# Performance work log

Hardware: AMD Instinct MI355X
Metric: run time of the kernel (lower is better)

Reference implementation:

```python
import jax, jax.numpy as jnp
import numpy as np


def swish(x):
    return x * jax.nn.sigmoid(x)


def setup_inputs() -> dict:
    key = jax.random.key(0)
    ks = jax.random.split(key, 12)
    b, n, c, h, dg, hid = 4, 512, 256, 8, 6, 16

    def lin(k, i, o):
        return jax.random.normal(k, (i, o), jnp.float32) / np.float32(np.sqrt(i))

    return {
        "pairwise_g": jax.random.normal(ks[0], (b, n, n, dg), jnp.float32),
        "coset_functions": jax.random.normal(ks[1], (b, n, c), jnp.float32),
        "fc_q_w": lin(ks[2], c, c), "fc_q_b": jnp.zeros((c,), jnp.float32),
        "fc_k_w": lin(ks[3], c, c), "fc_k_b": jnp.zeros((c,), jnp.float32),
        "in_w": lin(ks[4], c, c), "in_b": jnp.zeros((c,), jnp.float32),
        "out_w": lin(ks[5], c, c), "out_b": jnp.zeros((c,), jnp.float32),
        "loc_w1": jax.random.normal(ks[6], (h, dg, hid), jnp.float32) / np.float32(np.sqrt(dg)),
        "loc_b1": jnp.zeros((h, hid), jnp.float32),
        "loc_w2": jax.random.normal(ks[7], (h, hid, hid), jnp.float32) / np.float32(np.sqrt(hid)),
        "loc_b2": jnp.zeros((h, hid), jnp.float32),
        "loc_w3": jax.random.normal(ks[8], (h, hid, 1), jnp.float32) / np.float32(np.sqrt(hid)),
        "loc_b3": jnp.zeros((h, 1), jnp.float32),
        "mask": jax.random.randint(ks[9], (4, 512), 0, 2) > 0,
    }


def reference(pairwise_g, coset_functions, fc_q_w, fc_q_b, fc_k_w, fc_k_b,
              in_w, in_b, out_w, out_b,
              loc_w1, loc_b1, loc_w2, loc_b2, loc_w3, loc_b3, mask):
    # nbhd_idx = arange(n) in the original (dense neighborhoods), so all
    # advanced-index gathers are identities and are expressed as broadcasts.
    b, n, c = coset_functions.shape
    h = loc_w1.shape[0]
    d = c // h

    # DotProductKernel: scores scaled by sqrt(embed_dim) = sqrt(c)
    Q = (coset_functions @ fc_q_w + fc_q_b).reshape(b, n, h, d)
    K = (coset_functions @ fc_k_w + fc_k_b).reshape(b, n, h, d)
    A_feat = jnp.einsum('bnhd,bmhd->bnmh', Q, K) / np.float32(np.sqrt(c))  # (b,n,m,h)

    # MultiheadWeightNet location kernel: per-head 3-layer MLP with swish
    # after every linear (LieConv-style LinearBNact blocks), out_dim=1.
    x = swish(jnp.einsum('bnmg,hgk->bnmhk', pairwise_g, loc_w1) + loc_b1)
    x = swish(jnp.einsum('bnmhk,hkj->bnmhj', x, loc_w2) + loc_b2)
    A_loc = swish(jnp.einsum('bnmhk,hko->bnmho', x, loc_w3) + loc_b3)[..., 0]  # (b,n,m,h)

    pre = A_loc + A_feat
    nbhd_mask = mask[:, None, :, None]          # mask over keys j: (b,1,m,1)
    pre = jnp.where(nbhd_mask, pre, jnp.float32(-1e38))
    att = jax.nn.softmax(pre, axis=2)           # softmax over neighbor dim m

    V = (coset_functions @ in_w + in_b).reshape(b, n, h, d)  # input_linear
    out = jnp.einsum('bnmh,bmhd->bnhd', att, V).reshape(b, n, c)
    return out @ out_w + out_b                  # output_linear; (b,n,c_out)
```

## Files before the change

### kernel.cpp

```cpp
#include <hip/hip_runtime.h>
#include <math.h>

namespace {

constexpr int kB = 4, kN = 512, kC = 256, kH = 8, kDG = 6, kHID = 16;

constexpr int S_QH = 20;
constexpr int S_BT = 20;
constexpr int S_AT = 516;

typedef _Float16 half2v __attribute__((ext_vector_type(2)));
typedef _Float16 half4v __attribute__((ext_vector_type(4)));
typedef float float4v __attribute__((ext_vector_type(4)));
typedef unsigned uint2v __attribute__((ext_vector_type(2)));

__device__ __forceinline__ float swishf(float x) {
    return x * __builtin_amdgcn_rcpf(1.0f + __expf(-x));
}

__device__ __forceinline__ unsigned pk16(float a, float b) {
    unsigned short ha = __builtin_bit_cast(unsigned short, (_Float16)a);
    unsigned short hb = __builtin_bit_cast(unsigned short, (_Float16)b);
    return (unsigned)ha | ((unsigned)hb << 16);
}

__device__ __forceinline__ unsigned pkrtz(float a, float b) {
    return __builtin_bit_cast(unsigned, __builtin_amdgcn_cvt_pkrtz(a, b));
}

__device__ __forceinline__ float4v mfma16(half4v a, half4v b, float4v c) {
    return __builtin_amdgcn_mfma_f32_16x16x16f16(a, b, c, 0, 0, 0);
}

__global__ __launch_bounds__(256) void k_qkvc(
    const float* __restrict__ x,
    const float* __restrict__ wq, const float* __restrict__ bq,
    const float* __restrict__ wk, const float* __restrict__ bk,
    const float* __restrict__ wv, const float* __restrict__ bv,
    unsigned* __restrict__ Qh, unsigned* __restrict__ Kh,
    unsigned* __restrict__ Vh,
    const unsigned char* __restrict__ mraw,
    int* __restrict__ list, int* __restrict__ meta) {
    const int t = threadIdx.x;

    if (blockIdx.x == 256) {
        __shared__ int s_isbool;
        if (t == 0) s_isbool = 0;
        __syncthreads();
        int found = 0;
        for (int i = t; i < kB * kN; i += 256)
            if ((i & 3) && mraw[i]) found = 1;
        if (found) atomicOr(&s_isbool, 1);
        __syncthreads();
        const int isb = s_isbool;
        const int b = t >> 6, lane = t & 63;
        const int* mi = (const int*)mraw;
        int base = 0;
        for (int c = 0; c < 8; ++c) {
            const int m = c * 64 + lane;
            const int idx = b * kN + m;
            const int valid = isb ? (mraw[idx] != 0) : (mi[idx] != 0);
            unsigned long long bal = __ballot(valid);
            int rank = (int)__popcll(bal & ((1ull << lane) - 1ull));
            if (valid) list[b * kN + base + rank] = m;
            base += (int)__popcll(bal);
        }
        for (int i = base + lane; i < kN; i += 64)
            list[b * kN + i] = (base == 0) ? i : 0;
        if (lane == 0) {
            meta[b] = (base == 0) ? kN : base;
            meta[4 + b] = (base == 0);
        }
        return;
    }

    __shared__ float sx[8][kC];
    const int r0 = blockIdx.x * 8;
    #pragma unroll
    for (int r = 0; r < 8; ++r) sx[r][t] = x[(r0 + r) * kC + t];
    __syncthreads();
    float aq[8] = {}, ak[8] = {}, av[8] = {};
    for (int k = 0; k < kC; ++k) {
        const float q = wq[k * kC + t];
        const float kk = wk[k * kC + t];
        const float v = wv[k * kC + t];
        #pragma unroll
        for (int r = 0; r < 8; ++r) {
            aq[r] += sx[r][k] * q;
            ak[r] += sx[r][k] * kk;
            av[r] += sx[r][k] * v;
        }
    }
    const float qb = bq[t], kb = bk[t], vb = bv[t];
    #pragma unroll
    for (int r = 0; r < 8; ++r) {
        const float qv = aq[r] + qb;
        const float kv = ak[r] + kb;
        const float vv = av[r] + vb;
        const float qn = __shfl_down(qv, 1);
        const float kn = __shfl_down(kv, 1);
        const float vn = __shfl_down(vv, 1);
        if ((t & 1) == 0) {
            Qh[(r0 + r) * (kC / 2) + (t >> 1)] = pk16(qv, qn);
            Kh[(r0 + r) * (kC / 2) + (t >> 1)] = pk16(kv, kn);
            Vh[(r0 + r) * (kC / 2) + (t >> 1)] = pk16(vv, vn);
        }
    }
}

__global__ __launch_bounds__(256, 4) void k_attn(
    const float* __restrict__ G,
    const unsigned* __restrict__ Qh,
    const unsigned* __restrict__ Kh,
    const unsigned* __restrict__ Vh,
    const float* __restrict__ w1, const float* __restrict__ b1,
    const float* __restrict__ w2, const float* __restrict__ b2,
    const float* __restrict__ w3, const float* __restrict__ b3,
    const int* __restrict__ list, const int* __restrict__ meta,
    float* __restrict__ out) {
    __shared__ __align__(16) unsigned sQh[kH * S_QH];
    __shared__ __align__(16) uint4 sG4[kN];
    __shared__ int sList[kN];
    __shared__ __align__(16) float sB1T[kH * S_BT];
    __shared__ __align__(16) float sB2T[kH * S_BT];
    __shared__ __align__(16) float sW3T[kH * S_BT];
    __shared__ float sB3[kH];
    __shared__ float sAtt[kH * S_AT];
    __shared__ float sInv[kH];

    const int bn = blockIdx.x;
    const int b = bn >> 9;
    const int t = threadIdx.x;
    const int l = t & 63;
    const int p = l & 15;
    const int s = l >> 4;
    const int wid = t >> 6;

    half4v a1f[kH], a2f[kH];
    #pragma unroll
    for (int h = 0; h < kH; ++h) {
        #pragma unroll
        for (int r = 0; r < 4; ++r) {
            const int k = 4 * s + r;
            a1f[h][r] = (k < kDG) ? (_Float16)w1[(h * kDG + k) * kHID + p]
                                  : (_Float16)0.f;
            a2f[h][r] = (_Float16)w2[(h * kHID + k) * kHID + p];
        }
    }

    if (t < kH * S_QH) {
        const int hh = t / S_QH, r = t % S_QH;
        sQh[t] = (r < 16) ? Qh[bn * (kC / 2) + hh * 16 + r] : 0u;
    }
    sList[t] = list[b * kN + t];
    sList[t + 256] = list[b * kN + t + 256];
    #pragma unroll 1
    for (int rep = 0; rep < 2; ++rep) {
        const int m = t + rep * 256;
        const float* gp = G + ((size_t)bn * kN + m) * kDG;
        uint4 gw;
        gw.x = pkrtz(gp[0], gp[1]);
        gw.y = pkrtz(gp[2], gp[3]);
        gw.z = pkrtz(gp[4], gp[5]);
        gw.w = 0;
        sG4[m] = gw;
    }
    if (t < 128) {
        const int hh = t >> 4, j = t & 15;
        sB1T[hh * S_BT + j] = b1[hh * kHID + j];
        sB2T[hh * S_BT + j] = b2[hh * kHID + j];
        sW3T[hh * S_BT + j] = w3[hh * kHID + j];
        if (j == 0) sB3[hh] = b3[hh];
    }
    const int nv = meta[b];
    const int allm = meta[4 + b];
    __syncthreads();

    const unsigned* khB = Kh + (size_t)(b * kN) * (kC / 2);
    const int ntiles = (nv + 15) >> 4;

    #pragma unroll
    for (int h = 0; h < kH; ++h) {
        const float4v bv1 = *(const float4v*)&sB1T[h * S_BT + s * 4];
        const float4v bv2 = *(const float4v*)&sB2T[h * S_BT + s * 4];
        const float4v w3f = *(const float4v*)&sW3T[h * S_BT + s * 4];
        half4v w3h;
        #pragma unroll
        for (int r = 0; r < 4; ++r) w3h[r] = (_Float16)w3f[r];
        const float b3s = sB3[h];
        const float4v b3v = {b3s, b3s, b3s, b3s};
        const uint2v q0u = {sQh[h * S_QH + 2 * s], sQh[h * S_QH + 2 * s + 1]};
        const uint2v q1u = {sQh[h * S_QH + 8 + 2 * s], sQh[h * S_QH + 9 + 2 * s]};
        const half4v qA0 = __builtin_bit_cast(half4v, q0u);
        const half4v qA1 = __builtin_bit_cast(half4v, q1u);

        #pragma unroll 1
        for (int tile = wid; tile < ntiles; tile += 4) {
            const int mcw = tile * 16 + p;
            const int mc = min(mcw, nv - 1);
            const int m = sList[mc];
            const unsigned* gp = (const unsigned*)&sG4[m];
            uint2v gu = {gp[(s & 1) * 2], gp[(s & 1) * 2 + 1]};
            if (s >= 2) { gu[0] = 0u; gu[1] = 0u; }
            const half4v bg = __builtin_bit_cast(half4v, gu);
            const float4v c1 = mfma16(a1f[h], bg, bv1);
            const uint2v x1u = {pkrtz(swishf(c1[0]), swishf(c1[1])),
                                pkrtz(swishf(c1[2]), swishf(c1[3]))};
            const float4v c2 = mfma16(a2f[h], __builtin_bit_cast(half4v, x1u), bv2);
            const uint2v x2u = {pkrtz(swishf(c2[0]), swishf(c2[1])),
                                pkrtz(swishf(c2[2]), swishf(c2[3]))};
            const float4v c3 = mfma16(w3h, __builtin_bit_cast(half4v, x2u), b3v);
            const unsigned* kr = khB + (size_t)m * (kC / 2) + h * 16 + 2 * s;
            const uint2v k0 = {kr[0], kr[1]};
            const uint2v k1 = {kr[8], kr[9]};
            float4v ca = {0.f, 0.f, 0.f, 0.f};
            ca = mfma16(qA0, __builtin_bit_cast(half4v, k0), ca);
            ca = mfma16(qA1, __builtin_bit_cast(half4v, k1), ca);
            const float pre = swishf(c3[0]) + ca[0] * 0.0625f;
            if (s == 0 && mcw < nv)
                sAtt[h * S_AT + mcw] = allm ? 0.f : pre;
        }
    }
    __syncthreads();

    {
        const int hg = t >> 5;
        const int lane = t & 31;
        float mx = -3.4e38f;
        for (int idx = lane; idx < nv; idx += 32)
            mx = fmaxf(mx, sAtt[hg * S_AT + idx]);
        #pragma unroll
        for (int off = 16; off; off >>= 1)
            mx = fmaxf(mx, __shfl_xor(mx, off));
        float ls = 0.f;
        for (int idx = lane; idx < nv; idx += 32) {
            const float e = __expf(sAtt[hg * S_AT + idx] - mx);
            sAtt[hg * S_AT + idx] = e;
            ls += e;
        }
        #pragma unroll
        for (int off = 16; off; off >>= 1)
            ls += __shfl_xor(ls, off);
        if (lane == 0) sInv[hg] = 1.0f / ls;
    }
    __syncthreads();

    {
        const int hg = t >> 5;
        const int dp = (t >> 1) & 15;
        const int par = t & 1;
        const unsigned* vbp = Vh + (size_t)(b * kN) * (kC / 2) + hg * 16 + dp;
        float alo = 0.f, ahi = 0.f, blo = 0.f, bhi = 0.f;
        int mc = par;
        for (; mc + 2 < nv; mc += 4) {
            const float aw0 = sAtt[hg * S_AT + mc];
            const float aw1 = sAtt[hg * S_AT + mc + 2];
            const half2v v0 = __builtin_bit_cast(half2v, vbp[(size_t)sList[mc] * (kC / 2)]);
            const half2v v1 = __builtin_bit_cast(half2v, vbp[(size_t)sList[mc + 2] * (kC / 2)]);
            alo += aw0 * (float)v0[0];
            ahi += aw0 * (float)v0[1];
            blo += aw1 * (float)v1[0];
            bhi += aw1 * (float)v1[1];
        }
        for (; mc < nv; mc += 2) {
            const float aw = sAtt[hg * S_AT + mc];
            const half2v vv = __builtin_bit_cast(half2v, vbp[(size_t)sList[mc] * (kC / 2)]);
            alo += aw * (float)vv[0];
            ahi += aw * (float)vv[1];
        }
        alo += blo; ahi += bhi;
        alo += __shfl_xor(alo, 1);
        ahi += __shfl_xor(ahi, 1);
        out[bn * kC + t] = (par ? ahi : alo) * sInv[hg];
    }
}

__global__ __launch_bounds__(256) void k_proj(
    const float* __restrict__ x,
    const float* __restrict__ w, const float* __restrict__ bias,
    float* __restrict__ y) {
    __shared__ float sx[8][kC];
    const int r0 = blockIdx.x * 8;
    const int t = threadIdx.x;
    #pragma unroll
    for (int r = 0; r < 8; ++r) sx[r][t] = x[(r0 + r) * kC + t];
    __syncthreads();
    float acc[8] = {};
    for (int k = 0; k < kC; ++k) {
        const float wv = w[k * kC + t];
        #pragma unroll
        for (int r = 0; r < 8; ++r) acc[r] += sx[r][k] * wv;
    }
    const float bb = bias[t];
    #pragma unroll
    for (int r = 0; r < 8; ++r) y[(r0 + r) * kC + t] = acc[r] + bb;
}

}

extern "C" void kernel_launch(void* const* d_in, const int* in_sizes, int n_in,
                              void* d_out, int out_size, void* d_ws, size_t ws_size,
                              hipStream_t stream) {
    (void)in_sizes; (void)n_in; (void)out_size; (void)ws_size;
    const float* G  = (const float*)d_in[0];
    const float* cf = (const float*)d_in[1];
    const float* wq = (const float*)d_in[2];
    const float* bq = (const float*)d_in[3];
    const float* wk = (const float*)d_in[4];
    const float* bk = (const float*)d_in[5];
    const float* wv = (const float*)d_in[6];
    const float* bv = (const float*)d_in[7];
    const float* wo = (const float*)d_in[8];
    const float* bo = (const float*)d_in[9];
    const float* w1 = (const float*)d_in[10];
    const float* b1 = (const float*)d_in[11];
    const float* w2 = (const float*)d_in[12];
    const float* b2 = (const float*)d_in[13];
    const float* w3 = (const float*)d_in[14];
    const float* b3 = (const float*)d_in[15];
    const unsigned char* mraw = (const unsigned char*)d_in[16];

    const int rows = kB * kN;
    unsigned* Qh = (unsigned*)d_ws;
    unsigned* Kh = Qh + (size_t)rows * (kC / 2);
    unsigned* Vh = Kh + (size_t)rows * (kC / 2);
    float* O = (float*)(Vh + (size_t)rows * (kC / 2));
    int* list = (int*)(O + (size_t)rows * kC);
    int* meta = list + rows;

    k_qkvc<<<257, 256, 0, stream>>>(cf, wq, bq, wk, bk, wv, bv,
                                    Qh, Kh, Vh, mraw, list, meta);
    k_attn<<<rows, 256, 0, stream>>>(G, Qh, Kh, Vh, w1, b1, w2, b2, w3, b3,
                                     list, meta, O);
    k_proj<<<rows / 8, 256, 0, stream>>>(O, wo, bo, (float*)d_out);
}
```

Before: 264.1 us.

## Split projection kernels across column halves and interleave two tiles in attention loop

The QKV and output projection kernels now launch twice as many blocks, each handling 128 output columns for 4 rows per thread group, which raises grid parallelism on a large GPU. The attention score loop processes two 16-key tiles per iteration with interleaved MFMA chains and hoisted K loads, exposing more instruction-level parallelism to hide latency. The cost is more register pressure in the attention kernel and duplicated x loads across the column-split blocks.

```diff
diff --git a/kernel.cpp b/kernel.cpp
--- a/kernel.cpp
+++ b/kernel.cpp
@@ -43,7 +43,7 @@
     int* __restrict__ list, int* __restrict__ meta) {
     const int t = threadIdx.x;
 
-    if (blockIdx.x == 256) {
+    if (blockIdx.x == 512) {
         __shared__ int s_isbool;
         if (t == 0) s_isbool = 0;
         __syncthreads();
@@ -75,25 +75,30 @@
     }
 
     __shared__ float sx[8][kC];
-    const int r0 = blockIdx.x * 8;
+    const int r0 = (blockIdx.x >> 1) * 8;
+    const int c0 = (blockIdx.x & 1) * 128;
+    const int col = t & 127;
+    const int g = t >> 7;
     #pragma unroll
     for (int r = 0; r < 8; ++r) sx[r][t] = x[(r0 + r) * kC + t];
     __syncthreads();
-    float aq[8] = {}, ak[8] = {}, av[8] = {};
+    float aq[4] = {}, ak[4] = {}, av[4] = {};
     for (int k = 0; k < kC; ++k) {
-        const float q = wq[k * kC + t];
-        const float kk = wk[k * kC + t];
-        const float v = wv[k * kC + t];
-        #pragma unroll
-        for (int r = 0; r < 8; ++r) {
-            aq[r] += sx[r][k] * q;
-            ak[r] += sx[r][k] * kk;
-            av[r] += sx[r][k] * v;
-        }
-    }
-    const float qb = bq[t], kb = bk[t], vb = bv[t];
-    #pragma unroll
-    for (int r = 0; r < 8; ++r) {
+        const float q = wq[k * kC + c0 + col];
+        const float kk = wk[k * kC + c0 + col];
+        const float v = wv[k * kC + c0 + col];
+        #pragma unroll
+        for (int r = 0; r < 4; ++r) {
+            const float xs = sx[g * 4 + r][k];
+            aq[r] += xs * q;
+            ak[r] += xs * kk;
+            av[r] += xs * v;
+        }
+    }
+    const float qb = bq[c0 + col], kb = bk[c0 + col], vb = bv[c0 + col];
+    #pragma unroll
+    for (int r = 0; r < 4; ++r) {
+        const int row = r0 + g * 4 + r;
         const float qv = aq[r] + qb;
         const float kv = ak[r] + kb;
         const float vv = av[r] + vb;
@@ -101,9 +106,10 @@
         const float kn = __shfl_down(kv, 1);
         const float vn = __shfl_down(vv, 1);
         if ((t & 1) == 0) {
-            Qh[(r0 + r) * (kC / 2) + (t >> 1)] = pk16(qv, qn);
-            Kh[(r0 + r) * (kC / 2) + (t >> 1)] = pk16(kv, kn);
-            Vh[(r0 + r) * (kC / 2) + (t >> 1)] = pk16(vv, vn);
+            const int ci = (c0 + col) >> 1;
+            Qh[row * (kC / 2) + ci] = pk16(qv, qn);
+            Kh[row * (kC / 2) + ci] = pk16(kv, kn);
+            Vh[row * (kC / 2) + ci] = pk16(vv, vn);
         }
     }
 }
@@ -195,30 +201,50 @@
         const half4v qA1 = __builtin_bit_cast(half4v, q1u);
 
         #pragma unroll 1
-        for (int tile = wid; tile < ntiles; tile += 4) {
-            const int mcw = tile * 16 + p;
-            const int mc = min(mcw, nv - 1);
-            const int m = sList[mc];
-            const unsigned* gp = (const unsigned*)&sG4[m];
-            uint2v gu = {gp[(s & 1) * 2], gp[(s & 1) * 2 + 1]};
-            if (s >= 2) { gu[0] = 0u; gu[1] = 0u; }
-            const half4v bg = __builtin_bit_cast(half4v, gu);
-            const float4v c1 = mfma16(a1f[h], bg, bv1);
-            const uint2v x1u = {pkrtz(swishf(c1[0]), swishf(c1[1])),
-                                pkrtz(swishf(c1[2]), swishf(c1[3]))};
-            const float4v c2 = mfma16(a2f[h], __builtin_bit_cast(half4v, x1u), bv2);
-            const uint2v x2u = {pkrtz(swishf(c2[0]), swishf(c2[1])),
-                                pkrtz(swishf(c2[2]), swishf(c2[3]))};
-            const float4v c3 = mfma16(w3h, __builtin_bit_cast(half4v, x2u), b3v);
-            const unsigned* kr = khB + (size_t)m * (kC / 2) + h * 16 + 2 * s;
-            const uint2v k0 = {kr[0], kr[1]};
-            const uint2v k1 = {kr[8], kr[9]};
-            float4v ca = {0.f, 0.f, 0.f, 0.f};
-            ca = mfma16(qA0, __builtin_bit_cast(half4v, k0), ca);
-            ca = mfma16(qA1, __builtin_bit_cast(half4v, k1), ca);
-            const float pre = swishf(c3[0]) + ca[0] * 0.0625f;
-            if (s == 0 && mcw < nv)
-                sAtt[h * S_AT + mcw] = allm ? 0.f : pre;
+        for (int tile = wid; tile < ntiles; tile += 8) {
+            const int mcwA = tile * 16 + p;
+            const int mcwB = mcwA + 64;
+            const int mcA = min(mcwA, nv - 1);
+            const int mcB = min(mcwB, nv - 1);
+            const int mA = sList[mcA];
+            const int mB = sList[mcB];
+            const unsigned* krA = khB + (size_t)mA * (kC / 2) + h * 16 + 2 * s;
+            const unsigned* krB = khB + (size_t)mB * (kC / 2) + h * 16 + 2 * s;
+            const uint2v k0A = {krA[0], krA[1]};
+            const uint2v k1A = {krA[8], krA[9]};
+            const uint2v k0B = {krB[0], krB[1]};
+            const uint2v k1B = {krB[8], krB[9]};
+            const unsigned* gpA = (const unsigned*)&sG4[mA];
+            const unsigned* gpB = (const unsigned*)&sG4[mB];
+            uint2v guA = {gpA[(s & 1) * 2], gpA[(s & 1) * 2 + 1]};
+            uint2v guB = {gpB[(s & 1) * 2], gpB[(s & 1) * 2 + 1]};
+            if (s >= 2) { guA[0] = 0u; guA[1] = 0u; guB[0] = 0u; guB[1] = 0u; }
+            const half4v bgA = __builtin_bit_cast(half4v, guA);
+            const half4v bgB = __builtin_bit_cast(half4v, guB);
+            float4v caA = {0.f, 0.f, 0.f, 0.f};
+            float4v caB = {0.f, 0.f, 0.f, 0.f};
+            caA = mfma16(qA0, __builtin_bit_cast(half4v, k0A), caA);
+            caB = mfma16(qA0, __builtin_bit_cast(half4v, k0B), caB);
+            caA = mfma16(qA1, __builtin_bit_cast(half4v, k1A), caA);
+            caB = mfma16(qA1, __builtin_bit_cast(half4v, k1B), caB);
+            const float4v c1A = mfma16(a1f[h], bgA, bv1);
+            const float4v c1B = mfma16(a1f[h], bgB, bv1);
+            const uint2v x1uA = {pkrtz(swishf(c1A[0]), swishf(c1A[1])),
+                                 pkrtz(swishf(c1A[2]), swishf(c1A[3]))};
+            const uint2v x1uB = {pkrtz(swishf(c1B[0]), swishf(c1B[1])),
+                                 pkrtz(swishf(c1B[2]), swishf(c1B[3]))};
+            const float4v c2A = mfma16(a2f[h], __builtin_bit_cast(half4v, x1uA), bv2);
+            const float4v c2B = mfma16(a2f[h], __builtin_bit_cast(half4v, x1uB), bv2);
+            const uint2v x2uA = {pkrtz(swishf(c2A[0]), swishf(c2A[1])),
+                                 pkrtz(swishf(c2A[2]), swishf(c2A[3]))};
+            const uint2v x2uB = {pkrtz(swishf(c2B[0]), swishf(c2B[1])),
+                                 pkrtz(swishf(c2B[2]), swishf(c2B[3]))};
+            const float4v c3A = mfma16(w3h, __builtin_bit_cast(half4v, x2uA), b3v);
+            const float4v c3B = mfma16(w3h, __builtin_bit_cast(half4v, x2uB), b3v);
+            const float preA = swishf(c3A[0]) + caA[0] * 0.0625f;
+            const float preB = swishf(c3B[0]) + caB[0] * 0.0625f;
+            if (s == 0 && mcwA < nv) sAtt[h * S_AT + mcwA] = allm ? 0.f : preA;
+            if (s == 0 && mcwB < nv) sAtt[h * S_AT + mcwB] = allm ? 0.f : preB;
         }
     }
     __syncthreads();
@@ -280,20 +306,24 @@
     const float* __restrict__ w, const float* __restrict__ bias,
     float* __restrict__ y) {
     __shared__ float sx[8][kC];
-    const int r0 = blockIdx.x * 8;
     const int t = threadIdx.x;
+    const int r0 = (blockIdx.x >> 1) * 8;
+    const int c0 = (blockIdx.x & 1) * 128;
+    const int col = t & 127;
+    const int g = t >> 7;
     #pragma unroll
     for (int r = 0; r < 8; ++r) sx[r][t] = x[(r0 + r) * kC + t];
     __syncthreads();
-    float acc[8] = {};
+    float acc[4] = {};
     for (int k = 0; k < kC; ++k) {
-        const float wv = w[k * kC + t];
-        #pragma unroll
-        for (int r = 0; r < 8; ++r) acc[r] += sx[r][k] * wv;
-    }
-    const float bb = bias[t];
-    #pragma unroll
-    for (int r = 0; r < 8; ++r) y[(r0 + r) * kC + t] = acc[r] + bb;
+        const float wv = w[k * kC + c0 + col];
+        #pragma unroll
+        for (int r = 0; r < 4; ++r) acc[r] += sx[g * 4 + r][k] * wv;
+    }
+    const float bb = bias[c0 + col];
+    #pragma unroll
+    for (int r = 0; r < 4; ++r)
+        y[(r0 + g * 4 + r) * kC + c0 + col] = acc[r] + bb;
 }
 
 }
@@ -328,9 +358,9 @@
     int* list = (int*)(O + (size_t)rows * kC);
     int* meta = list + rows;
 
-    k_qkvc<<<257, 256, 0, stream>>>(cf, wq, bq, wk, bk, wv, bv,
+    k_qkvc<<<513, 256, 0, stream>>>(cf, wq, bq, wk, bk, wv, bv,
                                     Qh, Kh, Vh, mraw, list, meta);
     k_attn<<<rows, 256, 0, stream>>>(G, Qh, Kh, Vh, w1, b1, w2, b2, w3, b3,
                                      list, meta, O);
-    k_proj<<<rows / 8, 256, 0, stream>>>(O, wo, bo, (float*)d_out);
-}
+    k_proj<<<512, 256, 0, stream>>>(O, wo, bo, (float*)d_out);
+}
```

Result: no change. 268.8 us (+1.8%).
